# Optimization experiments

Measured on AMD Instinct MI355X. Metric: run time of the kernel, lower is better.

The kernel has to match this reference:

```python
import jax, jax.numpy as jnp
import numpy as np

B, S, D = 4, 4096, 256


def setup_inputs() -> dict:
    key = jax.random.key(0)
    k1, k2, k3, k4, k5 = jax.random.split(key, 5)
    query = jax.random.normal(k1, (B, S, D), dtype=jnp.float32)
    key_t = jax.random.normal(k2, (B, S, D), dtype=jnp.float32)
    value = jax.random.normal(k3, (B, S, D), dtype=jnp.float32)
    # nn.Linear(dim_model, dim_model): weight [D, D] (out, in), bias [D]
    bound = 1.0 / np.sqrt(D)
    Wq = jax.random.uniform(k4, (D, D), dtype=jnp.float32, minval=-bound, maxval=bound)
    bq = jax.random.uniform(k5, (D,), dtype=jnp.float32, minval=-bound, maxval=bound)
    return {"query": query, "key": key_t, "value": value, "Wq": Wq, "bq": bq}


def reference(query, key, value, Wq, bq):
    # Faithful to source: self.q is applied to ALL THREE inputs (source bug).
    q = jnp.einsum('bsd,od->bso', query, Wq) + bq  # [B,S,D]
    k = jnp.einsum('bsd,od->bso', key, Wq) + bq
    v = jnp.einsum('bsd,od->bso', value, Wq) + bq
    scale = jnp.sqrt(jnp.asarray(q.shape[-1], q.dtype))
    scores = jnp.einsum('bqd,bkd->bqk', q, k) / scale  # [B,S,S]
    attn = jax.nn.softmax(scores, axis=-1)
    return jnp.einsum('bqk,bkd->bqd', attn, v)  # [B,S,D]
```

## Files before the change

kernel.cpp:

```cpp
#include <hip/hip_runtime.h>


typedef __attribute__((ext_vector_type(4)))  float    f32x4;
typedef __attribute__((ext_vector_type(16))) float    f32x16;
typedef __attribute__((ext_vector_type(8)))  short    s16x8;
typedef __attribute__((ext_vector_type(2)))  unsigned u32x2;

#define AS_GLB const __attribute__((address_space(1))) unsigned
#define AS_LDS __attribute__((address_space(3))) unsigned

static constexpr float CEXP = 0.09016844f;
static constexpr float CM   = -32.0f * 0.09016844f;

static constexpr size_t QBF_OFF = 0;
static constexpr size_t KBF_OFF = 8ull  << 20;
static constexpr size_t VTB_OFF = 16ull << 20;
static constexpr size_t OT_OFF  = 24ull << 20;
static constexpr size_t LS_OFF  = 56ull << 20;

__device__ __forceinline__ unsigned bf16_rne(float f) {
  union { float f; unsigned u; } v; v.f = f;
  return (v.u + 0x7FFFu + ((v.u >> 16) & 1u)) >> 16;
}
__device__ __forceinline__ unsigned pkbf16(float a, float b) {
  return bf16_rne(a) | (bf16_rne(b) << 16);
}

__global__ __launch_bounds__(256, 2) void proj_kernel(
    const float* __restrict__ Xq, const float* __restrict__ Xk,
    const float* __restrict__ Xv, const float* __restrict__ Wq,
    const float* __restrict__ bq, char* __restrict__ ws)
{
  __shared__ char plds[32768];
  const int tid = threadIdx.x;
  const int lane = tid & 63, w = tid >> 6;
  const int wr = w >> 1, wc = w & 1;
  const int l15 = lane & 15, l4 = (lane >> 4) & 3;

  const int mt = blockIdx.x;
  const int tensor = mt >> 7;
  const int r0 = (mt & 127) << 7;
  const int n0 = blockIdx.y << 7;
  const float* A = (tensor == 0) ? Xq : (tensor == 1 ? Xk : Xv);

  f32x4 acc[4][4];
#pragma unroll
  for (int i = 0; i < 4; ++i)
#pragma unroll
    for (int j = 0; j < 4; ++j) { acc[i][j][0]=0.f; acc[i][j][1]=0.f; acc[i][j][2]=0.f; acc[i][j][3]=0.f; }

  for (int kt = 0; kt < 4; ++kt) {
    const int k0 = kt << 6;
#pragma unroll
    for (int j = 0; j < 8; ++j) {
      int c = j * 256 + tid;
      int row = c >> 4, col4 = c & 15;
      f32x4 av = *(const f32x4*)(A + (size_t)(r0 + row) * 256 + k0 + col4 * 4);
      u32x2 pa; pa[0] = pkbf16(av[0], av[1]); pa[1] = pkbf16(av[2], av[3]);
      int off = row * 128 + ((col4 * 8) ^ ((row & 7) << 4));
      *(u32x2*)(plds + off) = pa;
      f32x4 wv = *(const f32x4*)(Wq + (size_t)(n0 + row) * 256 + k0 + col4 * 4);
      u32x2 pw; pw[0] = pkbf16(wv[0], wv[1]); pw[1] = pkbf16(wv[2], wv[3]);
      *(u32x2*)(plds + 16384 + off) = pw;
    }
    __syncthreads();
#pragma unroll
    for (int ks = 0; ks < 2; ++ks) {
      s16x8 af[4], wf[4];
#pragma unroll
      for (int mi = 0; mi < 4; ++mi) {
        int row = wr * 64 + mi * 16 + l15;
        af[mi] = *(const s16x8*)(plds + row * 128 + ((ks * 64 + l4 * 16) ^ ((row & 7) << 4)));
      }
#pragma unroll
      for (int ni = 0; ni < 4; ++ni) {
        int row = wc * 64 + ni * 16 + l15;
        wf[ni] = *(const s16x8*)(plds + 16384 + row * 128 + ((ks * 64 + l4 * 16) ^ ((row & 7) << 4)));
      }
      if (tensor == 1) {
#pragma unroll
        for (int mi = 0; mi < 4; ++mi)
#pragma unroll
          for (int ni = 0; ni < 4; ++ni)
            acc[mi][ni] = __builtin_amdgcn_mfma_f32_16x16x32_bf16(wf[ni], af[mi], acc[mi][ni], 0, 0, 0);
      } else {
#pragma unroll
        for (int mi = 0; mi < 4; ++mi)
#pragma unroll
          for (int ni = 0; ni < 4; ++ni)
            acc[mi][ni] = __builtin_amdgcn_mfma_f32_16x16x32_bf16(af[mi], wf[ni], acc[mi][ni], 0, 0, 0);
      }
    }
    __syncthreads();
  }

  if (tensor == 0) {
    unsigned short* Qb = (unsigned short*)(ws + QBF_OFF);
#pragma unroll
    for (int ni = 0; ni < 4; ++ni) {
      int gn = n0 + wc * 64 + ni * 16 + l15;
      float bias = bq[gn];
#pragma unroll
      for (int mi = 0; mi < 4; ++mi) {
        int mrow = r0 + wr * 64 + mi * 16 + l4 * 4;
#pragma unroll
        for (int j = 0; j < 4; ++j)
          Qb[(size_t)(mrow + j) * 256 + gn] = (unsigned short)bf16_rne(acc[mi][ni][j] + bias);
      }
    }
  } else if (tensor == 1) {
    char* Kf = ws + KBF_OFF;
#pragma unroll
    for (int ni = 0; ni < 4; ++ni) {
      int dbase = n0 + wc * 64 + ni * 16 + l4 * 4;
      f32x4 bv = *(const f32x4*)(bq + dbase);
#pragma unroll
      for (int mi = 0; mi < 4; ++mi) {
        int s = r0 + wr * 64 + mi * 16 + l15;
        int b2 = s >> 12, sl = s & 31, kb = (s & 4095) >> 5;
        size_t chunk = (((size_t)b2 * 128 + kb) * 32 + (dbase >> 3)) * 32 + sl;
        u32x2 pv;
        pv[0] = pkbf16(acc[mi][ni][0] + bv[0], acc[mi][ni][1] + bv[1]);
        pv[1] = pkbf16(acc[mi][ni][2] + bv[2], acc[mi][ni][3] + bv[3]);
        *(u32x2*)(Kf + chunk * 16 + (dbase & 7) * 2) = pv;
      }
    }
  } else {
    char* Vf = ws + VTB_OFF;
#pragma unroll
    for (int ni = 0; ni < 4; ++ni) {
      int gn = n0 + wc * 64 + ni * 16 + l15;
      float bias = bq[gn];
#pragma unroll
      for (int mi = 0; mi < 4; ++mi) {
        int s = r0 + wr * 64 + mi * 16 + l4 * 4;
        int b2 = s >> 12, kb = (s & 4095) >> 5, sl = s & 31;
        size_t chunk = ((((size_t)b2 * 128 + kb) * 4 + (sl >> 3)) * 8 + (gn >> 5)) * 32 + (gn & 31);
        u32x2 pv;
        pv[0] = pkbf16(acc[mi][ni][0] + bias, acc[mi][ni][1] + bias);
        pv[1] = pkbf16(acc[mi][ni][2] + bias, acc[mi][ni][3] + bias);
        *(u32x2*)(Vf + chunk * 16 + (sl & 7) * 2) = pv;
      }
    }
  }
}

__global__ __launch_bounds__(256, 2) void flash_kernel(char* __restrict__ ws)
{
  __shared__ char lds[65536];
  const int tid = threadIdx.x;
  const int lane = tid & 63, w = tid >> 6;
  const int l31 = lane & 31, h = lane >> 5;

  const int bid  = blockIdx.x;
  const int sp   = bid & 3;
  const int b    = (bid >> 2) & 3;
  const int qblk = bid >> 4;
  const int q0w  = qblk * 128 + w * 32;
  const int kb0  = sp * 32;

  const char* Kfb = ws + KBF_OFF + (size_t)b * (2u << 20);
  const char* Vfb = ws + VTB_OFF + (size_t)b * (2u << 20);

  s16x8 qf[16];
  {
    const char* qrow = ws + QBF_OFF + (size_t)((b << 12) + q0w + l31) * 512 + h * 16;
#pragma unroll
    for (int i = 0; i < 16; ++i) qf[i] = *(const s16x8*)(qrow + i * 32);
  }
#pragma unroll
  for (int i = 0; i < 16; ++i) asm volatile("" :: "v"(qf[i]));

  f32x16 O[8];
#pragma unroll
  for (int t8 = 0; t8 < 8; ++t8)
#pragma unroll
    for (int r = 0; r < 16; ++r) O[t8][r] = 0.f;

  float l_run = 0.f;
  s16x8 paP0, paP1;

  auto STAGE_K = [&](int buf, int t) {
    const char* ksrc = Kfb + (size_t)(kb0 + t) * 16384;
#pragma unroll
    for (int i = 0; i < 4; ++i) {
      unsigned c = (unsigned)(w * 4 + i) << 10;
      __builtin_amdgcn_global_load_lds((AS_GLB*)(ksrc + c + (unsigned)lane * 16),
          (AS_LDS*)(lds + buf * 16384 + c), 16, 0, 0);
    }
  };
  auto STAGE_V = [&](int buf, int t) {
    const char* vsrc = Vfb + (size_t)(kb0 + t) * 16384;
#pragma unroll
    for (int i = 0; i < 4; ++i) {
      unsigned c = (unsigned)(w * 4 + i) << 10;
      __builtin_amdgcn_global_load_lds((AS_GLB*)(vsrc + c + (unsigned)lane * 16),
          (AS_LDS*)(lds + 32768 + buf * 16384 + c), 16, 0, 0);
    }
  };

  auto SOFTMAX_PACK = [&](const f32x16& pe, const f32x16& po) {
    float p[16];
#pragma unroll
    for (int r = 0; r < 16; ++r)
      p[r] = __builtin_exp2f(__builtin_fmaf(pe[r] + po[r], CEXP, CM));
    float s0 = (p[0] + p[1]) + (p[2] + p[3]);
    float s1 = (p[4] + p[5]) + (p[6] + p[7]);
    float s2 = (p[8] + p[9]) + (p[10] + p[11]);
    float s3 = (p[12] + p[13]) + (p[14] + p[15]);
    l_run += (s0 + s1) + (s2 + s3);
    unsigned a0, a1, b0, b1, c0, c1, d0, d1;
    asm("v_cvt_pk_bf16_f32 %0, %1, %2" : "=v"(a0) : "v"(p[0]),  "v"(p[1]));
    asm("v_cvt_pk_bf16_f32 %0, %1, %2" : "=v"(a1) : "v"(p[2]),  "v"(p[3]));
    asm("v_cvt_pk_bf16_f32 %0, %1, %2" : "=v"(b0) : "v"(p[4]),  "v"(p[5]));
    asm("v_cvt_pk_bf16_f32 %0, %1, %2" : "=v"(b1) : "v"(p[6]),  "v"(p[7]));
    asm("v_cvt_pk_bf16_f32 %0, %1, %2" : "=v"(c0) : "v"(p[8]),  "v"(p[9]));
    asm("v_cvt_pk_bf16_f32 %0, %1, %2" : "=v"(c1) : "v"(p[10]), "v"(p[11]));
    asm("v_cvt_pk_bf16_f32 %0, %1, %2" : "=v"(d0) : "v"(p[12]), "v"(p[13]));
    asm("v_cvt_pk_bf16_f32 %0, %1, %2" : "=v"(d1) : "v"(p[14]), "v"(p[15]));
    asm("v_permlane32_swap_b32 %0, %1" : "+v"(a0), "+v"(b0));
    asm("v_permlane32_swap_b32 %0, %1" : "+v"(a1), "+v"(b1));
    asm("v_permlane32_swap_b32 %0, %1" : "+v"(c0), "+v"(d0));
    asm("v_permlane32_swap_b32 %0, %1" : "+v"(c1), "+v"(d1));
    union { s16x8 v; unsigned u[4]; } u0, u1;
    u0.u[0] = a0; u0.u[1] = a1; u0.u[2] = b0; u0.u[3] = b1;
    u1.u[0] = c0; u1.u[1] = c1; u1.u[2] = d0; u1.u[3] = d1;
    paP0 = u0.v; paP1 = u1.v;
  };

  STAGE_K(0, 0);
  asm volatile("s_waitcnt vmcnt(0)" ::: "memory");
  __builtin_amdgcn_s_barrier();
  __builtin_amdgcn_sched_barrier(0);

  {
    STAGE_K(1, 1);
    STAGE_V(0, 0);
    const char* kb = lds;
    f32x16 pe, po;
#pragma unroll
    for (int r = 0; r < 16; ++r) { pe[r] = 0.f; po[r] = 0.f; }
    __builtin_amdgcn_s_setprio(1);
#pragma unroll
    for (int i = 0; i < 16; i += 2) {
      s16x8 kf0 = *(const s16x8*)(kb + ((2 * i + h) << 9) + l31 * 16);
      pe = __builtin_amdgcn_mfma_f32_32x32x16_bf16(kf0, qf[i], pe, 0, 0, 0);
      s16x8 kf1 = *(const s16x8*)(kb + ((2 * (i + 1) + h) << 9) + l31 * 16);
      po = __builtin_amdgcn_mfma_f32_32x32x16_bf16(kf1, qf[i + 1], po, 0, 0, 0);
    }
    __builtin_amdgcn_s_setprio(0);
    SOFTMAX_PACK(pe, po);
    asm volatile("s_waitcnt vmcnt(0)" ::: "memory");
    __builtin_amdgcn_s_barrier();
    __builtin_amdgcn_sched_barrier(0);
  }

  for (int t = 1; t < 32; ++t) {
    if (t < 31) STAGE_K((t + 1) & 1, t + 1);
    STAGE_V(t & 1, t);
    const char* kb  = lds + (t & 1) * 16384;
    const char* vbp = lds + 32768 + ((t + 1) & 1) * 16384;
    f32x16 pe, po;
#pragma unroll
    for (int r = 0; r < 16; ++r) { pe[r] = 0.f; po[r] = 0.f; }
    __builtin_amdgcn_s_setprio(1);
#pragma unroll
    for (int i = 0; i < 8; ++i) {
      s16x8 kf0 = *(const s16x8*)(kb + ((4 * i + h) << 9) + l31 * 16);
      pe = __builtin_amdgcn_mfma_f32_32x32x16_bf16(kf0, qf[2 * i], pe, 0, 0, 0);
      s16x8 vv0 = *(const s16x8*)(vbp + ((h * 8 + i) << 9) + l31 * 16);
      O[i] = __builtin_amdgcn_mfma_f32_32x32x16_bf16(paP0, vv0, O[i], 0, 0, 0);
      s16x8 kf1 = *(const s16x8*)(kb + ((4 * i + 2 + h) << 9) + l31 * 16);
      po = __builtin_amdgcn_mfma_f32_32x32x16_bf16(kf1, qf[2 * i + 1], po, 0, 0, 0);
      s16x8 vv1 = *(const s16x8*)(vbp + (((2 + h) * 8 + i) << 9) + l31 * 16);
      O[i] = __builtin_amdgcn_mfma_f32_32x32x16_bf16(paP1, vv1, O[i], 0, 0, 0);
    }
    __builtin_amdgcn_s_setprio(0);
    SOFTMAX_PACK(pe, po);
    asm volatile("s_waitcnt vmcnt(0)" ::: "memory");
    __builtin_amdgcn_s_barrier();
    __builtin_amdgcn_sched_barrier(0);
  }

  {
    const char* vb = lds + 32768 + 16384;
    __builtin_amdgcn_s_setprio(1);
#pragma unroll
    for (int t8 = 0; t8 < 8; ++t8) {
      s16x8 v0 = *(const s16x8*)(vb + ((h * 8 + t8) << 9) + l31 * 16);
      O[t8] = __builtin_amdgcn_mfma_f32_32x32x16_bf16(paP0, v0, O[t8], 0, 0, 0);
      s16x8 v1 = *(const s16x8*)(vb + (((2 + h) * 8 + t8) << 9) + l31 * 16);
      O[t8] = __builtin_amdgcn_mfma_f32_32x32x16_bf16(paP1, v1, O[t8], 0, 0, 0);
    }
    __builtin_amdgcn_s_setprio(0);
  }

  l_run += __shfl_xor(l_run, 32, 64);

  unsigned short* OTb = (unsigned short*)(ws + OT_OFF) +
                        (((size_t)(sp * 4 + b) << 12) << 8);
#pragma unroll
  for (int t8 = 0; t8 < 8; ++t8) {
    int d = t8 * 32 + l31;
#pragma unroll
    for (int r = 0; r < 16; ++r) {
      int q = q0w + (r & 3) + 8 * (r >> 2) + 4 * h;
      OTb[(size_t)q * 256 + d] = (unsigned short)bf16_rne(O[t8][r]);
    }
  }
  if (lane < 32) {
    int idx = ((sp * 4 + b) << 12) + q0w + l31;
    ((float*)(ws + LS_OFF))[idx] = l_run;
  }
}

__global__ __launch_bounds__(256) void merge_kernel(const char* __restrict__ ws,
                                                    float* __restrict__ out)
{
  const int t = threadIdx.x;
  const int b = blockIdx.x;
  const int s0 = blockIdx.y << 4;
  const int soff = t >> 7, dd = (t & 127) * 2;
  const unsigned short* OTb = (const unsigned short*)(ws + OT_OFF);
  const float* Ls = (const float*)(ws + LS_OFF);
  for (int si = 0; si < 8; ++si) {
    int s = s0 + si * 2 + soff;
    float L = 0.f;
#pragma unroll
    for (int sp = 0; sp < 4; ++sp) L += Ls[((sp * 4 + b) << 12) + s];
    float rL = 1.0f / L;
    float a0 = 0.f, a1 = 0.f;
#pragma unroll
    for (int sp = 0; sp < 4; ++sp) {
      unsigned uv = *(const unsigned*)(OTb + ((((size_t)(sp * 4 + b) << 12) + s) << 8) + dd);
      union { unsigned u; float f; } lo, hi;
      lo.u = uv << 16; hi.u = uv & 0xFFFF0000u;
      a0 += lo.f; a1 += hi.f;
    }
    float2 o; o.x = a0 * rL; o.y = a1 * rL;
    *(float2*)(out + (((size_t)(b << 12) + s) << 8) + dd) = o;
  }
}

extern "C" void kernel_launch(void* const* d_in, const int* in_sizes, int n_in,
                              void* d_out, int out_size, void* d_ws, size_t ws_size,
                              hipStream_t stream) {
  const float* q  = (const float*)d_in[0];
  const float* k  = (const float*)d_in[1];
  const float* v  = (const float*)d_in[2];
  const float* Wq = (const float*)d_in[3];
  const float* bq = (const float*)d_in[4];
  char* ws = (char*)d_ws;
  float* out = (float*)d_out;
  hipLaunchKernelGGL(proj_kernel, dim3(384, 2), dim3(256), 0, stream, q, k, v, Wq, bq, ws);
  hipLaunchKernelGGL(flash_kernel, dim3(512), dim3(256), 0, stream, ws);
  hipLaunchKernelGGL(merge_kernel, dim3(4, 256), dim3(256), 0, stream, ws, out);
}
```

Baseline: 113.7 us.

## Restructure attention loop with partial vmcnt waits and interleaved MFMA/softmax scheduling

Moves the wait for staged K/V tiles to the top of each iteration with a partial vmcnt, so the next tile's global-to-LDS loads stay in flight during compute instead of being drained at the end. Uses sched_group_barrier to interleave the QK and PV MFMAs with the softmax exp/pack VALU work and the LDS reads, overlapping matrix and vector pipes. It also peels the last iteration. The risk is a miscounted vmcnt, which could race on LDS buffers, and tight scheduling constraints that the compiler may not honour well.

Measured after the change: 112.2 us. Within noise of the previous version (-1.4%).

```diff
diff --git a/kernel.cpp b/kernel.cpp
--- a/kernel.cpp
+++ b/kernel.cpp
@@ -8,6 +8,7 @@
 
 #define AS_GLB const __attribute__((address_space(1))) unsigned
 #define AS_LDS __attribute__((address_space(3))) unsigned
+#define SGB    __builtin_amdgcn_sched_group_barrier
 
 static constexpr float CEXP = 0.09016844f;
 static constexpr float CM   = -32.0f * 0.09016844f;
@@ -199,6 +200,26 @@
     }
   };
 
+  auto QK = [&](const char* kb, f32x16& pe, f32x16& po) {
+#pragma unroll
+    for (int r = 0; r < 16; ++r) { pe[r] = 0.f; po[r] = 0.f; }
+#pragma unroll
+    for (int i = 0; i < 16; i += 2) {
+      s16x8 kf0 = *(const s16x8*)(kb + ((2 * i + h) << 9) + l31 * 16);
+      pe = __builtin_amdgcn_mfma_f32_32x32x16_bf16(kf0, qf[i], pe, 0, 0, 0);
+      s16x8 kf1 = *(const s16x8*)(kb + ((2 * (i + 1) + h) << 9) + l31 * 16);
+      po = __builtin_amdgcn_mfma_f32_32x32x16_bf16(kf1, qf[i + 1], po, 0, 0, 0);
+    }
+  };
+  auto PV = [&](const char* vb) {
+#pragma unroll
+    for (int t8 = 0; t8 < 8; ++t8) {
+      s16x8 v0 = *(const s16x8*)(vb + ((h * 8 + t8) << 9) + l31 * 16);
+      O[t8] = __builtin_amdgcn_mfma_f32_32x32x16_bf16(paP0, v0, O[t8], 0, 0, 0);
+      s16x8 v1 = *(const s16x8*)(vb + (((2 + h) * 8 + t8) << 9) + l31 * 16);
+      O[t8] = __builtin_amdgcn_mfma_f32_32x32x16_bf16(paP1, v1, O[t8], 0, 0, 0);
+    }
+  };
   auto SOFTMAX_PACK = [&](const f32x16& pe, const f32x16& po) {
     float p[16];
 #pragma unroll
@@ -236,62 +257,59 @@
   {
     STAGE_K(1, 1);
     STAGE_V(0, 0);
-    const char* kb = lds;
     f32x16 pe, po;
-#pragma unroll
-    for (int r = 0; r < 16; ++r) { pe[r] = 0.f; po[r] = 0.f; }
     __builtin_amdgcn_s_setprio(1);
-#pragma unroll
-    for (int i = 0; i < 16; i += 2) {
-      s16x8 kf0 = *(const s16x8*)(kb + ((2 * i + h) << 9) + l31 * 16);
-      pe = __builtin_amdgcn_mfma_f32_32x32x16_bf16(kf0, qf[i], pe, 0, 0, 0);
-      s16x8 kf1 = *(const s16x8*)(kb + ((2 * (i + 1) + h) << 9) + l31 * 16);
-      po = __builtin_amdgcn_mfma_f32_32x32x16_bf16(kf1, qf[i + 1], po, 0, 0, 0);
-    }
+    QK(lds, pe, po);
+    __builtin_amdgcn_s_setprio(0);
+    SOFTMAX_PACK(pe, po);
+    __builtin_amdgcn_s_barrier();
+    __builtin_amdgcn_sched_barrier(0);
+  }
+
+  for (int t = 1; t < 31; ++t) {
+    STAGE_K((t + 1) & 1, t + 1);
+    STAGE_V(t & 1, t);
+    asm volatile("s_waitcnt vmcnt(8)" ::: "memory");
+    __builtin_amdgcn_s_barrier();
+    __builtin_amdgcn_sched_barrier(0);
+
+    const char* kb = lds + (t & 1) * 16384;
+    const char* vb = lds + 32768 + ((t + 1) & 1) * 16384;
+    f32x16 pe, po;
+    __builtin_amdgcn_s_setprio(1);
+    QK(kb, pe, po);
+    PV(vb);
+    SOFTMAX_PACK(pe, po);
+    SGB(0x100, 6, 0);
+#pragma unroll
+    for (int i = 0; i < 16; ++i) { SGB(0x8, 1, 0); SGB(0x100, 1, 0); }
+#pragma unroll
+    for (int i = 0; i < 10; ++i) { SGB(0x8, 1, 0); SGB(0x100, 1, 0); SGB(0x2, 4, 0); }
+#pragma unroll
+    for (int i = 0; i < 6; ++i)  { SGB(0x8, 1, 0); SGB(0x2, 4, 0); }
+    __builtin_amdgcn_s_setprio(0);
+    __builtin_amdgcn_s_barrier();
+    __builtin_amdgcn_sched_barrier(0);
+  }
+
+  {
+    STAGE_V(1, 31);
+    asm volatile("s_waitcnt vmcnt(4)" ::: "memory");
+    __builtin_amdgcn_s_barrier();
+    __builtin_amdgcn_sched_barrier(0);
+    const char* kb = lds + 16384;
+    const char* vb = lds + 32768;
+    f32x16 pe, po;
+    __builtin_amdgcn_s_setprio(1);
+    QK(kb, pe, po);
+    PV(vb);
     __builtin_amdgcn_s_setprio(0);
     SOFTMAX_PACK(pe, po);
     asm volatile("s_waitcnt vmcnt(0)" ::: "memory");
     __builtin_amdgcn_s_barrier();
     __builtin_amdgcn_sched_barrier(0);
-  }
-
-  for (int t = 1; t < 32; ++t) {
-    if (t < 31) STAGE_K((t + 1) & 1, t + 1);
-    STAGE_V(t & 1, t);
-    const char* kb  = lds + (t & 1) * 16384;
-    const char* vbp = lds + 32768 + ((t + 1) & 1) * 16384;
-    f32x16 pe, po;
-#pragma unroll
-    for (int r = 0; r < 16; ++r) { pe[r] = 0.f; po[r] = 0.f; }
     __builtin_amdgcn_s_setprio(1);
-#pragma unroll
-    for (int i = 0; i < 8; ++i) {
-      s16x8 kf0 = *(const s16x8*)(kb + ((4 * i + h) << 9) + l31 * 16);
-      pe = __builtin_amdgcn_mfma_f32_32x32x16_bf16(kf0, qf[2 * i], pe, 0, 0, 0);
-      s16x8 vv0 = *(const s16x8*)(vbp + ((h * 8 + i) << 9) + l31 * 16);
-      O[i] = __builtin_amdgcn_mfma_f32_32x32x16_bf16(paP0, vv0, O[i], 0, 0, 0);
-      s16x8 kf1 = *(const s16x8*)(kb + ((4 * i + 2 + h) << 9) + l31 * 16);
-      po = __builtin_amdgcn_mfma_f32_32x32x16_bf16(kf1, qf[2 * i + 1], po, 0, 0, 0);
-      s16x8 vv1 = *(const s16x8*)(vbp + (((2 + h) * 8 + i) << 9) + l31 * 16);
-      O[i] = __builtin_amdgcn_mfma_f32_32x32x16_bf16(paP1, vv1, O[i], 0, 0, 0);
-    }
-    __builtin_amdgcn_s_setprio(0);
-    SOFTMAX_PACK(pe, po);
-    asm volatile("s_waitcnt vmcnt(0)" ::: "memory");
-    __builtin_amdgcn_s_barrier();
-    __builtin_amdgcn_sched_barrier(0);
-  }
-
-  {
-    const char* vb = lds + 32768 + 16384;
-    __builtin_amdgcn_s_setprio(1);
-#pragma unroll
-    for (int t8 = 0; t8 < 8; ++t8) {
-      s16x8 v0 = *(const s16x8*)(vb + ((h * 8 + t8) << 9) + l31 * 16);
-      O[t8] = __builtin_amdgcn_mfma_f32_32x32x16_bf16(paP0, v0, O[t8], 0, 0, 0);
-      s16x8 v1 = *(const s16x8*)(vb + (((2 + h) * 8 + t8) << 9) + l31 * 16);
-      O[t8] = __builtin_amdgcn_mfma_f32_32x32x16_bf16(paP1, v1, O[t8], 0, 0, 0);
-    }
+    PV(lds + 32768 + 16384);
     __builtin_amdgcn_s_setprio(0);
   }
 
```
